# Optimization experiments

Measured on AMD Instinct MI355X. Metric: run time of the kernel, lower is better.

## Reference

```python
import jax, jax.numpy as jnp
import numpy as np

BLOCK_LEN = 64

def _segsum(x):
    # x: (..., T) -> (..., T, T) with entry [t, s] = sum_{u=s+1..t} x[u], -inf above diagonal
    T = x.shape[-1]
    cs = jnp.cumsum(x, axis=-1)
    ss = cs[..., :, None] - cs[..., None, :]
    mask = jnp.tril(jnp.ones((T, T), dtype=bool))
    return jnp.where(mask, ss, -jnp.inf)

def setup_inputs() -> dict:
    key = jax.random.key(0)
    kx, ka, kb, kc = jax.random.split(key, 4)
    b, L, h, p, n = 4, 4096, 32, 64, 16
    X = jax.random.normal(kx, (b, L, h, p), dtype=jnp.float32)
    # negative, small-magnitude A so exp(cumsum(A)) stays finite (decaying SSM),
    # matching the math of the module while keeping the baseline numerically sane
    A = -0.1 * jnp.abs(jax.random.normal(ka, (b, L, h), dtype=jnp.float32))
    B = jax.random.normal(kb, (b, L, h, n), dtype=jnp.float32)
    C = jax.random.normal(kc, (b, L, h, n), dtype=jnp.float32)
    return {"X": X, "A": A, "B": B, "C": C}

def reference(X, A, B, C):
    b, L, h, p = X.shape
    n = B.shape[-1]
    l = BLOCK_LEN
    c = L // l
    # chunk into blocks
    Xb = X.reshape(b, c, l, h, p)                       # b c l h p
    Ab = A.reshape(b, c, l, h).transpose(0, 3, 1, 2)    # b h c l
    Bb = B.reshape(b, c, l, h, n)                       # b c l h n
    Cb = C.reshape(b, c, l, h, n)                       # b c l h n
    A_cumsum = jnp.cumsum(Ab, axis=-1)                  # b h c l
    # intra-chunk (diagonal) term; equals the fused per-timestep scan
    # h_t = exp(A_t)*h_{t-1} + B_t*x_t ; y_t = C_t . h_t
    Lmat = jnp.exp(_segsum(Ab))                         # b h c l l (lower-tri)
    Y_diag = jnp.einsum('bclhn,bcshn,bhcls,bcshp->bclhp', Cb, Bb, Lmat, Xb)
    # per-chunk end states
    decay_states = jnp.exp(A_cumsum[..., -1:] - A_cumsum)  # b h c l
    states = jnp.einsum('bclhn,bhcl,bclhp->bchpn', Bb, decay_states, Xb)
    states = jnp.concatenate([jnp.zeros_like(states[:, :1]), states], axis=1)  # b (c+1) h p n
    # inter-chunk recurrence via segment-sum of chunk totals
    decay_chunk = jnp.exp(_segsum(jnp.pad(A_cumsum[..., -1], ((0, 0), (0, 0), (1, 0)))))  # b h (c+1) (c+1)
    new_states = jnp.einsum('bhzc,bchpn->bzhpn', decay_chunk, states)
    states = new_states[:, :-1]                          # b c h p n
    # state -> output contribution
    state_decay_out = jnp.exp(A_cumsum)                  # b h c l
    Y_off = jnp.einsum('bclhn,bchpn,bhcl->bclhp', Cb, states, state_decay_out)
    return (Y_diag + Y_off).reshape(b, L, h, p)
```

## Files before the change

### kernel.cpp

```cpp
#include <hip/hip_runtime.h>

#define BATCH   4
#define SEQLEN  4096
#define NHEADS  32
#define PDIM    64
#define NDIM    16
#define CHUNK   64
#define NCHUNK  64

typedef short v8s __attribute__((ext_vector_type(8)));
typedef float v4f __attribute__((ext_vector_type(4)));

__device__ __forceinline__ short f2bf(float f) {
    union { float f; unsigned u; } x; x.f = f;
    unsigned r = (x.u + 0x7FFFu + ((x.u >> 16) & 1u)) >> 16;
    return (short)r;
}
__device__ __forceinline__ float bf2f(short s) {
    union { unsigned u; float f; } x; x.u = ((unsigned)(unsigned short)s) << 16;
    return x.f;
}

__device__ __forceinline__ float wave_iscan(float v, int lane) {
#pragma unroll
    for (int d = 1; d < 64; d <<= 1) {
        float o = __shfl_up(v, (unsigned)d, 64);
        if (lane >= d) v += o;
    }
    return v;
}

__global__ __launch_bounds__(256) void k_states(
    const float* __restrict__ X, const float* __restrict__ A,
    const float* __restrict__ Bm, float* __restrict__ states,
    float* __restrict__ csum)
{
    const int cc = blockIdx.x, hh = blockIdx.y, bb = blockIdx.z;
    const int tid = threadIdx.x;
    const int lane = tid & 63, W = tid >> 6;
    const int t0 = bb * SEQLEN + cc * CHUNK;

    __shared__ __align__(16) float sXraw[CHUNK][PDIM + 1];
    __shared__ __align__(16) short bF[1024];
    __shared__ float sDec[CHUNK];

    {
        const int sb = tid >> 4, p4 = (tid & 15) * 4;
        for (int i = 0; i < 4; ++i) {
            int s = sb + i * 16;
            const float4 v = *(const float4*)&X[((size_t)(t0 + s) * NHEADS + hh) * PDIM + p4];
            sXraw[s][p4]     = v.x; sXraw[s][p4 + 1] = v.y;
            sXraw[s][p4 + 2] = v.z; sXraw[s][p4 + 3] = v.w;
        }
    }
    {
        const int r = tid >> 2, n0 = (tid & 3) * 4;
        float4 bv = *(const float4*)&Bm[((size_t)(t0 + r) * NHEADS + hh) * NDIM + n0];
        const int kk = r >> 5, q = (r >> 3) & 3, j = r & 7;
        const int base = (kk * 64 + q * 16) * 8 + j;
        bF[base + (n0 + 0) * 8] = f2bf(bv.x);
        bF[base + (n0 + 1) * 8] = f2bf(bv.y);
        bF[base + (n0 + 2) * 8] = f2bf(bv.z);
        bF[base + (n0 + 3) * 8] = f2bf(bv.w);
    }
    if (tid < 64) {
        float a = A[(t0 + tid) * NHEADS + hh];
        float v = wave_iscan(a, lane);
        float tot = __shfl(v, 63, 64);
        sDec[tid] = __expf(tot - v);
        if (tid == 0) csum[(bb * NHEADS + hh) * NCHUNK + cc] = tot;
    }
    __syncthreads();

    const int m = lane & 15, q = lane >> 4;
    v8s a0, a1;
#pragma unroll
    for (int j = 0; j < 8; ++j) {
        const int tr = q * 8 + j;
        a0[j] = f2bf(sXraw[tr][W * 16 + m] * sDec[tr]);
        a1[j] = f2bf(sXraw[32 + tr][W * 16 + m] * sDec[32 + tr]);
    }
    v8s b0 = *(const v8s*)&bF[(0 * 64 + lane) * 8];
    v8s b1 = *(const v8s*)&bF[(1 * 64 + lane) * 8];
    const v4f zero = {0.f, 0.f, 0.f, 0.f};
    v4f acc = __builtin_amdgcn_mfma_f32_16x16x32_bf16(a0, b0, zero, 0, 0, 0);
    acc = __builtin_amdgcn_mfma_f32_16x16x32_bf16(a1, b1, acc, 0, 0, 0);

    const int n = lane & 15;
    float* sp = states + ((size_t)(bb * NHEADS + hh) * NCHUNK + cc) * (PDIM * NDIM);
#pragma unroll
    for (int r = 0; r < 4; ++r)
        sp[(W * 16 + q * 4 + r) * NDIM + n] = acc[r];
}

__global__ __launch_bounds__(256) void k_scan(
    float* __restrict__ states, const float* __restrict__ csum)
{
    const int bh = blockIdx.y;
    const int el = blockIdx.x * 256 + threadIdx.x;
    __shared__ float sE[NCHUNK];
    if (threadIdx.x < NCHUNK) sE[threadIdx.x] = __expf(csum[bh * NCHUNK + threadIdx.x]);
    __syncthreads();
    float* base = states + (size_t)bh * NCHUNK * (PDIM * NDIM) + el;
    float v[NCHUNK];
#pragma unroll
    for (int z = 0; z < NCHUNK; ++z) v[z] = base[z * (PDIM * NDIM)];
    float S = 0.f;
#pragma unroll
    for (int z = 0; z < NCHUNK; ++z) {
        const float nv = v[z];
        v[z] = S;
        S = sE[z] * S + nv;
    }
#pragma unroll
    for (int z = 0; z < NCHUNK; ++z) base[z * (PDIM * NDIM)] = v[z];
}

__global__ __launch_bounds__(256) void k_out(
    const float* __restrict__ X, const float* __restrict__ A,
    const float* __restrict__ Bm, const float* __restrict__ Cm,
    const float* __restrict__ states, float* __restrict__ Y)
{
    const int cc = blockIdx.x, hh = blockIdx.y, bb = blockIdx.z;
    const int tid = threadIdx.x;
    const int lane = tid & 63, W = tid >> 6;
    const int qq = lane >> 4, nn = lane & 15;
    const int t0 = bb * SEQLEN + cc * CHUNK;

    __shared__ __align__(16) char uBuf[CHUNK * (PDIM + 1) * 4];
    float (*sXraw)[PDIM + 1] = (float (*)[PDIM + 1])uBuf;
    short* gF = (short*)uBuf;
    __shared__ __align__(16) short xF[4096];
    __shared__ __align__(16) short cF[2048];
    __shared__ __align__(16) short bF[2048];
    __shared__ __align__(16) short sF[2048];
    __shared__ float sCum[CHUNK];

    {
        const int sb = tid >> 4, p4 = (tid & 15) * 4;
        for (int i = 0; i < 4; ++i) {
            int s = sb + i * 16;
            const float4 v = *(const float4*)&X[((size_t)(t0 + s) * NHEADS + hh) * PDIM + p4];
            sXraw[s][p4]     = v.x; sXraw[s][p4 + 1] = v.y;
            sXraw[s][p4 + 2] = v.z; sXraw[s][p4 + 3] = v.w;
        }
    }
    {
        const int r = tid >> 2, nn0 = (tid & 3) * 4;
        const int off = ((r >> 4) * 64 + (nn0 >> 3) * 16 + (r & 15)) * 8 + (nn0 & 7);
        float4 cv = *(const float4*)&Cm[((size_t)(t0 + r) * NHEADS + hh) * NDIM + nn0];
        cF[off] = f2bf(cv.x); cF[off + 1] = f2bf(cv.y);
        cF[off + 2] = f2bf(cv.z); cF[off + 3] = f2bf(cv.w);
        float4 bv = *(const float4*)&Bm[((size_t)(t0 + r) * NHEADS + hh) * NDIM + nn0];
        bF[off] = f2bf(bv.x); bF[off + 1] = f2bf(bv.y);
        bF[off + 2] = f2bf(bv.z); bF[off + 3] = f2bf(bv.w);
        const float* sp = states + ((size_t)(bb * NHEADS + hh) * NCHUNK + cc) * (PDIM * NDIM)
                                 + r * NDIM + nn0;
        float4 sv = *(const float4*)sp;
        sF[off] = f2bf(sv.x); sF[off + 1] = f2bf(sv.y);
        sF[off + 2] = f2bf(sv.z); sF[off + 3] = f2bf(sv.w);
    }
    {
        const v8s z8 = {0, 0, 0, 0, 0, 0, 0, 0};
        for (int z = tid; z < 384; z += 256) {
            short* base = (z < 128) ? cF : (z < 256) ? bF : sF;
            int idx = z & 127;
            int off = (idx >> 5) * 512 + 256 + (idx & 31) * 8;
            *(v8s*)&base[off] = z8;
        }
    }
    if (tid < 64) {
        float a = A[(t0 + tid) * NHEADS + hh];
        sCum[tid] = wave_iscan(a, lane);
    }
    __syncthreads();

    for (int c = tid; c < 512; c += 256) {
        int cn = c & 15, cq = (c >> 4) & 3, nt = (c >> 6) & 3, kk = c >> 8;
        int srow = kk * 32 + cq * 8, p = nt * 16 + cn;
        v8s v;
        for (int j = 0; j < 8; ++j) v[j] = f2bf(sXraw[srow + j][p]);
        *(v8s*)&xF[c * 8] = v;
    }
    __syncthreads();

    const v8s cfrag = *(const v8s*)&cF[(W * 64 + lane) * 8];
    const v4f zero = {0.f, 0.f, 0.f, 0.f};
    for (int st = 0; st < 4; ++st) {
        const int kk = st >> 1, q2 = (st & 1) * 2 + (nn >> 3), j2 = nn & 7;
        if (st <= W) {
            v8s bfrag = *(const v8s*)&bF[(st * 64 + lane) * 8];
            v4f acc = __builtin_amdgcn_mfma_f32_16x16x32_bf16(cfrag, bfrag, zero, 0, 0, 0);
            const int s = st * 16 + nn;
            const float cums = sCum[s];
            for (int r = 0; r < 4; ++r) {
                int t = W * 16 + qq * 4 + r;
                float g = (t >= s) ? acc[r] * __expf(sCum[t] - cums) : 0.f;
                gF[((W * 2 + kk) * 64 + q2 * 16 + qq * 4 + r) * 8 + j2] = f2bf(g);
            }
        } else if (kk == 0 || W >= 2) {
            for (int r = 0; r < 4; ++r)
                gF[((W * 2 + kk) * 64 + q2 * 16 + qq * 4 + r) * 8 + j2] = 0;
        }
    }
    const float et = __expf(sCum[W * 16 + nn]);
    v8s cefrag;
    for (int j = 0; j < 8; ++j) cefrag[j] = f2bf(bf2f(cfrag[j]) * et);
    __syncthreads();

    const v8s ga0 = *(const v8s*)&gF[((W * 2 + 0) * 64 + lane) * 8];
    const bool usekk1 = (W >= 2);
    v8s ga1 = {0, 0, 0, 0, 0, 0, 0, 0};
    if (usekk1) ga1 = *(const v8s*)&gF[((W * 2 + 1) * 64 + lane) * 8];
    v4f acc[4];
    for (int nt = 0; nt < 4; ++nt) {
        v8s sfrag = *(const v8s*)&sF[(nt * 64 + lane) * 8];
        v4f a = __builtin_amdgcn_mfma_f32_16x16x32_bf16(cefrag, sfrag, zero, 0, 0, 0);
        v8s x0 = *(const v8s*)&xF[((0 * 4 + nt) * 64 + lane) * 8];
        a = __builtin_amdgcn_mfma_f32_16x16x32_bf16(ga0, x0, a, 0, 0, 0);
        if (usekk1) {
            v8s x1 = *(const v8s*)&xF[((1 * 4 + nt) * 64 + lane) * 8];
            a = __builtin_amdgcn_mfma_f32_16x16x32_bf16(ga1, x1, a, 0, 0, 0);
        }
        acc[nt] = a;
    }
    for (int r = 0; r < 4; ++r) {
        int t = W * 16 + qq * 4 + r;
        float* yp = Y + ((size_t)(t0 + t) * NHEADS + hh) * PDIM + nn;
        for (int nt = 0; nt < 4; ++nt) yp[nt * 16] = acc[nt][r];
    }
}

extern "C" void kernel_launch(void* const* d_in, const int* in_sizes, int n_in,
                              void* d_out, int out_size, void* d_ws, size_t ws_size,
                              hipStream_t stream) {
    const float* X  = (const float*)d_in[0];
    const float* A  = (const float*)d_in[1];
    const float* Bm = (const float*)d_in[2];
    const float* Cm = (const float*)d_in[3];
    float* Y = (float*)d_out;

    float* states = (float*)d_ws;
    float* csum   = states + (size_t)BATCH * NHEADS * NCHUNK * PDIM * NDIM;

    dim3 grid(NCHUNK, NHEADS, BATCH);
    k_states<<<grid, 256, 0, stream>>>(X, A, Bm, states, csum);
    dim3 gscan(4, BATCH * NHEADS, 1);
    k_scan<<<gscan, 256, 0, stream>>>(states, csum);
    k_out<<<grid, 256, 0, stream>>>(X, A, Bm, Cm, states, Y);
}
```

Measured before the change: 335.0 us.

## Fuse state, scan and output kernels into one chunk-sequential double-buffered kernel

Replaces the three-kernel pipeline (per-chunk states, inter-chunk scan, output) with a single kernel in which each block owns one (batch, head, half of P) slice and walks the 64 chunks in order. The inter-chunk state is carried in registers and handed to the next chunk through shared memory, so the global workspace write and read of chunk states disappears. Four producer waves prefetch the next chunk's X, B, C and A into double-buffered shared memory while four consumer waves compute the current chunk. The cost is much less parallelism: only 256 blocks, each running a 64-step serial loop with a block barrier per step, so speed depends on hiding global load latency within each block.

```diff
diff --git a/kernel.cpp b/kernel.cpp
--- a/kernel.cpp
+++ b/kernel.cpp
@@ -7,6 +7,7 @@
 #define NDIM    16
 #define CHUNK   64
 #define NCHUNK  64
+#define PHALF   32
 
 typedef short v8s __attribute__((ext_vector_type(8)));
 typedef float v4f __attribute__((ext_vector_type(4)));
@@ -30,204 +31,162 @@
     return v;
 }
 
-__global__ __launch_bounds__(256) void k_states(
+__global__ __launch_bounds__(512) void k_fused(
     const float* __restrict__ X, const float* __restrict__ A,
-    const float* __restrict__ Bm, float* __restrict__ states,
-    float* __restrict__ csum)
+    const float* __restrict__ Bm, const float* __restrict__ Cm,
+    float* __restrict__ Y)
 {
-    const int cc = blockIdx.x, hh = blockIdx.y, bb = blockIdx.z;
+    const int ph = blockIdx.x, hh = blockIdx.y, bb = blockIdx.z;
     const int tid = threadIdx.x;
-    const int lane = tid & 63, W = tid >> 6;
-    const int t0 = bb * SEQLEN + cc * CHUNK;
-
-    __shared__ __align__(16) float sXraw[CHUNK][PDIM + 1];
-    __shared__ __align__(16) short bF[1024];
-    __shared__ float sDec[CHUNK];
+    const int lane = tid & 63;
+    const int wv = tid >> 6;
+    const int W = wv & 3;
+    const int qq = lane >> 4, nn = lane & 15;
+
+    __shared__ __align__(16) float sXraw[2][CHUNK][PHALF + 1];
+    __shared__ __align__(16) short cFq[2][2048];
+    __shared__ __align__(16) short bFq[2][2048];
+    __shared__ __align__(16) short bFs[2][1024];
+    __shared__ __align__(16) short sF [2][1024];
+    __shared__ __align__(16) short gF [4096];
+    __shared__ float araw[2][CHUNK];
 
     {
-        const int sb = tid >> 4, p4 = (tid & 15) * 4;
-        for (int i = 0; i < 4; ++i) {
-            int s = sb + i * 16;
-            const float4 v = *(const float4*)&X[((size_t)(t0 + s) * NHEADS + hh) * PDIM + p4];
-            sXraw[s][p4]     = v.x; sXraw[s][p4 + 1] = v.y;
-            sXraw[s][p4 + 2] = v.z; sXraw[s][p4 + 3] = v.w;
-        }
-    }
-    {
-        const int r = tid >> 2, n0 = (tid & 3) * 4;
-        float4 bv = *(const float4*)&Bm[((size_t)(t0 + r) * NHEADS + hh) * NDIM + n0];
-        const int kk = r >> 5, q = (r >> 3) & 3, j = r & 7;
-        const int base = (kk * 64 + q * 16) * 8 + j;
-        bF[base + (n0 + 0) * 8] = f2bf(bv.x);
-        bF[base + (n0 + 1) * 8] = f2bf(bv.y);
-        bF[base + (n0 + 2) * 8] = f2bf(bv.z);
-        bF[base + (n0 + 3) * 8] = f2bf(bv.w);
-    }
-    if (tid < 64) {
-        float a = A[(t0 + tid) * NHEADS + hh];
-        float v = wave_iscan(a, lane);
-        float tot = __shfl(v, 63, 64);
-        sDec[tid] = __expf(tot - v);
-        if (tid == 0) csum[(bb * NHEADS + hh) * NCHUNK + cc] = tot;
+        const v8s z8 = {0,0,0,0,0,0,0,0};
+        if (tid < 512) { ((v8s*)cFq)[tid] = z8; ((v8s*)bFq)[tid] = z8; }
+        if (tid < 256) ((v8s*)sF)[tid] = z8;
     }
     __syncthreads();
 
-    const int m = lane & 15, q = lane >> 4;
-    v8s a0, a1;
-#pragma unroll
-    for (int j = 0; j < 8; ++j) {
-        const int tr = q * 8 + j;
-        a0[j] = f2bf(sXraw[tr][W * 16 + m] * sDec[tr]);
-        a1[j] = f2bf(sXraw[32 + tr][W * 16 + m] * sDec[32 + tr]);
-    }
-    v8s b0 = *(const v8s*)&bF[(0 * 64 + lane) * 8];
-    v8s b1 = *(const v8s*)&bF[(1 * 64 + lane) * 8];
+    auto stage = [&](int c, int buf) {
+        const int ptid = tid & 255;
+        const int t0c = bb * SEQLEN + c * CHUNK;
+#pragma unroll
+        for (int i = 0; i < 2; ++i) {
+            const int idx = ptid + i * 256;
+            const int row = idx >> 3, p4 = (idx & 7) * 4;
+            const float4 v = *(const float4*)&X[((size_t)(t0c + row) * NHEADS + hh) * PDIM + ph * PHALF + p4];
+            sXraw[buf][row][p4 + 0] = v.x; sXraw[buf][row][p4 + 1] = v.y;
+            sXraw[buf][row][p4 + 2] = v.z; sXraw[buf][row][p4 + 3] = v.w;
+        }
+        {
+            const int r = ptid >> 2, n0 = (ptid & 3) * 4;
+            const float4 bv = *(const float4*)&Bm[((size_t)(t0c + r) * NHEADS + hh) * NDIM + n0];
+            const int offq = ((r >> 4) * 64 + (n0 >> 3) * 16 + (r & 15)) * 8 + (n0 & 7);
+            bFq[buf][offq + 0] = f2bf(bv.x); bFq[buf][offq + 1] = f2bf(bv.y);
+            bFq[buf][offq + 2] = f2bf(bv.z); bFq[buf][offq + 3] = f2bf(bv.w);
+            const int kk = r >> 5, q = (r >> 3) & 3, jj = r & 7;
+            const int bs = (kk * 64 + q * 16) * 8 + jj;
+            bFs[buf][bs + (n0 + 0) * 8] = f2bf(bv.x);
+            bFs[buf][bs + (n0 + 1) * 8] = f2bf(bv.y);
+            bFs[buf][bs + (n0 + 2) * 8] = f2bf(bv.z);
+            bFs[buf][bs + (n0 + 3) * 8] = f2bf(bv.w);
+            const float4 cv = *(const float4*)&Cm[((size_t)(t0c + r) * NHEADS + hh) * NDIM + n0];
+            cFq[buf][offq + 0] = f2bf(cv.x); cFq[buf][offq + 1] = f2bf(cv.y);
+            cFq[buf][offq + 2] = f2bf(cv.z); cFq[buf][offq + 3] = f2bf(cv.w);
+        }
+        if (ptid < CHUNK) araw[buf][ptid] = A[(size_t)(t0c + ptid) * NHEADS + hh];
+    };
+
+    if (wv >= 4) stage(0, 0);
+    __syncthreads();
+
+    v4f S = {0.f, 0.f, 0.f, 0.f};
     const v4f zero = {0.f, 0.f, 0.f, 0.f};
-    v4f acc = __builtin_amdgcn_mfma_f32_16x16x32_bf16(a0, b0, zero, 0, 0, 0);
-    acc = __builtin_amdgcn_mfma_f32_16x16x32_bf16(a1, b1, acc, 0, 0, 0);
-
-    const int n = lane & 15;
-    float* sp = states + ((size_t)(bb * NHEADS + hh) * NCHUNK + cc) * (PDIM * NDIM);
-#pragma unroll
-    for (int r = 0; r < 4; ++r)
-        sp[(W * 16 + q * 4 + r) * NDIM + n] = acc[r];
-}
-
-__global__ __launch_bounds__(256) void k_scan(
-    float* __restrict__ states, const float* __restrict__ csum)
-{
-    const int bh = blockIdx.y;
-    const int el = blockIdx.x * 256 + threadIdx.x;
-    __shared__ float sE[NCHUNK];
-    if (threadIdx.x < NCHUNK) sE[threadIdx.x] = __expf(csum[bh * NCHUNK + threadIdx.x]);
-    __syncthreads();
-    float* base = states + (size_t)bh * NCHUNK * (PDIM * NDIM) + el;
-    float v[NCHUNK];
-#pragma unroll
-    for (int z = 0; z < NCHUNK; ++z) v[z] = base[z * (PDIM * NDIM)];
-    float S = 0.f;
-#pragma unroll
-    for (int z = 0; z < NCHUNK; ++z) {
-        const float nv = v[z];
-        v[z] = S;
-        S = sE[z] * S + nv;
-    }
-#pragma unroll
-    for (int z = 0; z < NCHUNK; ++z) base[z * (PDIM * NDIM)] = v[z];
-}
-
-__global__ __launch_bounds__(256) void k_out(
-    const float* __restrict__ X, const float* __restrict__ A,
-    const float* __restrict__ Bm, const float* __restrict__ Cm,
-    const float* __restrict__ states, float* __restrict__ Y)
-{
-    const int cc = blockIdx.x, hh = blockIdx.y, bb = blockIdx.z;
-    const int tid = threadIdx.x;
-    const int lane = tid & 63, W = tid >> 6;
-    const int qq = lane >> 4, nn = lane & 15;
-    const int t0 = bb * SEQLEN + cc * CHUNK;
-
-    __shared__ __align__(16) char uBuf[CHUNK * (PDIM + 1) * 4];
-    float (*sXraw)[PDIM + 1] = (float (*)[PDIM + 1])uBuf;
-    short* gF = (short*)uBuf;
-    __shared__ __align__(16) short xF[4096];
-    __shared__ __align__(16) short cF[2048];
-    __shared__ __align__(16) short bF[2048];
-    __shared__ __align__(16) short sF[2048];
-    __shared__ float sCum[CHUNK];
-
-    {
-        const int sb = tid >> 4, p4 = (tid & 15) * 4;
-        for (int i = 0; i < 4; ++i) {
-            int s = sb + i * 16;
-            const float4 v = *(const float4*)&X[((size_t)(t0 + s) * NHEADS + hh) * PDIM + p4];
-            sXraw[s][p4]     = v.x; sXraw[s][p4 + 1] = v.y;
-            sXraw[s][p4 + 2] = v.z; sXraw[s][p4 + 3] = v.w;
+
+#pragma unroll 1
+    for (int k = 0; k < NCHUNK; ++k) {
+        const int cur = k & 1;
+        if (wv >= 4) {
+            if (k + 1 < NCHUNK) stage(k + 1, cur ^ 1);
+        } else {
+            const int t0c = bb * SEQLEN + k * CHUNK;
+            const float cum = wave_iscan(araw[cur][lane], lane);
+            const float tot = __shfl(cum, 63, 64);
+            float tcum[4];
+#pragma unroll
+            for (int r = 0; r < 4; ++r) tcum[r] = __shfl(cum, W * 16 + qq * 4 + r, 64);
+
+            const v8s cfrag = *(const v8s*)&cFq[cur][(W * 64 + lane) * 8];
+#pragma unroll
+            for (int st = 0; st < 4; ++st) {
+                const int kk = st >> 1, q2 = (st & 1) * 2 + (nn >> 3), j2 = nn & 7;
+                if (st <= W) {
+                    const v8s bfrag = *(const v8s*)&bFq[cur][(st * 64 + lane) * 8];
+                    v4f acc = __builtin_amdgcn_mfma_f32_16x16x32_bf16(cfrag, bfrag, zero, 0, 0, 0);
+                    const float cums = __shfl(cum, st * 16 + nn, 64);
+#pragma unroll
+                    for (int r = 0; r < 4; ++r) {
+                        const int t = W * 16 + qq * 4 + r;
+                        const int s = st * 16 + nn;
+                        const float g = (t >= s) ? acc[r] * __expf(tcum[r] - cums) : 0.f;
+                        gF[((W * 2 + kk) * 64 + q2 * 16 + qq * 4 + r) * 8 + j2] = f2bf(g);
+                    }
+                } else if (kk == 0 || W >= 2) {
+#pragma unroll
+                    for (int r = 0; r < 4; ++r)
+                        gF[((W * 2 + kk) * 64 + q2 * 16 + qq * 4 + r) * 8 + j2] = 0;
+                }
+            }
+            const float et = __expf(__shfl(cum, W * 16 + nn, 64));
+            v8s cefrag;
+#pragma unroll
+            for (int j = 0; j < 8; ++j) cefrag[j] = f2bf(bf2f(cfrag[j]) * et);
+
+            const v8s ga0 = *(const v8s*)&gF[((W * 2 + 0) * 64 + lane) * 8];
+            const bool usekk1 = (W >= 2);
+            v8s ga1 = {0, 0, 0, 0, 0, 0, 0, 0};
+            if (usekk1) ga1 = *(const v8s*)&gF[((W * 2 + 1) * 64 + lane) * 8];
+
+            v4f ya[2];
+#pragma unroll
+            for (int nt = 0; nt < 2; ++nt) {
+                const v8s sfrag = *(const v8s*)&sF[cur][(nt * 64 + lane) * 8];
+                v4f a = __builtin_amdgcn_mfma_f32_16x16x32_bf16(cefrag, sfrag, zero, 0, 0, 0);
+                v8s x0;
+#pragma unroll
+                for (int j = 0; j < 8; ++j) x0[j] = f2bf(sXraw[cur][qq * 8 + j][nt * 16 + nn]);
+                a = __builtin_amdgcn_mfma_f32_16x16x32_bf16(ga0, x0, a, 0, 0, 0);
+                if (usekk1) {
+                    v8s x1;
+#pragma unroll
+                    for (int j = 0; j < 8; ++j) x1[j] = f2bf(sXraw[cur][32 + qq * 8 + j][nt * 16 + nn]);
+                    a = __builtin_amdgcn_mfma_f32_16x16x32_bf16(ga1, x1, a, 0, 0, 0);
+                }
+                ya[nt] = a;
+            }
+#pragma unroll
+            for (int r = 0; r < 4; ++r) {
+                const int t = W * 16 + qq * 4 + r;
+                float* yp = Y + ((size_t)(t0c + t) * NHEADS + hh) * PDIM + ph * PHALF + nn;
+                yp[0]  = ya[0][r];
+                yp[16] = ya[1][r];
+            }
+
+            if (W < 2) {
+                v8s a0, a1;
+#pragma unroll
+                for (int j = 0; j < 8; ++j) {
+                    const int tr = qq * 8 + j;
+                    a0[j] = f2bf(sXraw[cur][tr][W * 16 + nn] *
+                                 __expf(tot - __shfl(cum, tr, 64)));
+                    a1[j] = f2bf(sXraw[cur][32 + tr][W * 16 + nn] *
+                                 __expf(tot - __shfl(cum, 32 + tr, 64)));
+                }
+                const v8s b0 = *(const v8s*)&bFs[cur][(0 * 64 + lane) * 8];
+                const v8s b1 = *(const v8s*)&bFs[cur][(1 * 64 + lane) * 8];
+                v4f sa = __builtin_amdgcn_mfma_f32_16x16x32_bf16(a0, b0, zero, 0, 0, 0);
+                sa = __builtin_amdgcn_mfma_f32_16x16x32_bf16(a1, b1, sa, 0, 0, 0);
+                const float Et = __expf(tot);
+#pragma unroll
+                for (int r = 0; r < 4; ++r) S[r] = Et * S[r] + sa[r];
+                short* d = &sF[cur ^ 1][0];
+#pragma unroll
+                for (int r = 0; r < 4; ++r)
+                    d[(W * 64 + (nn >> 3) * 16 + qq * 4 + r) * 8 + (nn & 7)] = f2bf(S[r]);
+            }
         }
-    }
-    {
-        const int r = tid >> 2, nn0 = (tid & 3) * 4;
-        const int off = ((r >> 4) * 64 + (nn0 >> 3) * 16 + (r & 15)) * 8 + (nn0 & 7);
-        float4 cv = *(const float4*)&Cm[((size_t)(t0 + r) * NHEADS + hh) * NDIM + nn0];
-        cF[off] = f2bf(cv.x); cF[off + 1] = f2bf(cv.y);
-        cF[off + 2] = f2bf(cv.z); cF[off + 3] = f2bf(cv.w);
-        float4 bv = *(const float4*)&Bm[((size_t)(t0 + r) * NHEADS + hh) * NDIM + nn0];
-        bF[off] = f2bf(bv.x); bF[off + 1] = f2bf(bv.y);
-        bF[off + 2] = f2bf(bv.z); bF[off + 3] = f2bf(bv.w);
-        const float* sp = states + ((size_t)(bb * NHEADS + hh) * NCHUNK + cc) * (PDIM * NDIM)
-                                 + r * NDIM + nn0;
-        float4 sv = *(const float4*)sp;
-        sF[off] = f2bf(sv.x); sF[off + 1] = f2bf(sv.y);
-        sF[off + 2] = f2bf(sv.z); sF[off + 3] = f2bf(sv.w);
-    }
-    {
-        const v8s z8 = {0, 0, 0, 0, 0, 0, 0, 0};
-        for (int z = tid; z < 384; z += 256) {
-            short* base = (z < 128) ? cF : (z < 256) ? bF : sF;
-            int idx = z & 127;
-            int off = (idx >> 5) * 512 + 256 + (idx & 31) * 8;
-            *(v8s*)&base[off] = z8;
-        }
-    }
-    if (tid < 64) {
-        float a = A[(t0 + tid) * NHEADS + hh];
-        sCum[tid] = wave_iscan(a, lane);
-    }
-    __syncthreads();
-
-    for (int c = tid; c < 512; c += 256) {
-        int cn = c & 15, cq = (c >> 4) & 3, nt = (c >> 6) & 3, kk = c >> 8;
-        int srow = kk * 32 + cq * 8, p = nt * 16 + cn;
-        v8s v;
-        for (int j = 0; j < 8; ++j) v[j] = f2bf(sXraw[srow + j][p]);
-        *(v8s*)&xF[c * 8] = v;
-    }
-    __syncthreads();
-
-    const v8s cfrag = *(const v8s*)&cF[(W * 64 + lane) * 8];
-    const v4f zero = {0.f, 0.f, 0.f, 0.f};
-    for (int st = 0; st < 4; ++st) {
-        const int kk = st >> 1, q2 = (st & 1) * 2 + (nn >> 3), j2 = nn & 7;
-        if (st <= W) {
-            v8s bfrag = *(const v8s*)&bF[(st * 64 + lane) * 8];
-            v4f acc = __builtin_amdgcn_mfma_f32_16x16x32_bf16(cfrag, bfrag, zero, 0, 0, 0);
-            const int s = st * 16 + nn;
-            const float cums = sCum[s];
-            for (int r = 0; r < 4; ++r) {
-                int t = W * 16 + qq * 4 + r;
-                float g = (t >= s) ? acc[r] * __expf(sCum[t] - cums) : 0.f;
-                gF[((W * 2 + kk) * 64 + q2 * 16 + qq * 4 + r) * 8 + j2] = f2bf(g);
-            }
-        } else if (kk == 0 || W >= 2) {
-            for (int r = 0; r < 4; ++r)
-                gF[((W * 2 + kk) * 64 + q2 * 16 + qq * 4 + r) * 8 + j2] = 0;
-        }
-    }
-    const float et = __expf(sCum[W * 16 + nn]);
-    v8s cefrag;
-    for (int j = 0; j < 8; ++j) cefrag[j] = f2bf(bf2f(cfrag[j]) * et);
-    __syncthreads();
-
-    const v8s ga0 = *(const v8s*)&gF[((W * 2 + 0) * 64 + lane) * 8];
-    const bool usekk1 = (W >= 2);
-    v8s ga1 = {0, 0, 0, 0, 0, 0, 0, 0};
-    if (usekk1) ga1 = *(const v8s*)&gF[((W * 2 + 1) * 64 + lane) * 8];
-    v4f acc[4];
-    for (int nt = 0; nt < 4; ++nt) {
-        v8s sfrag = *(const v8s*)&sF[(nt * 64 + lane) * 8];
-        v4f a = __builtin_amdgcn_mfma_f32_16x16x32_bf16(cefrag, sfrag, zero, 0, 0, 0);
-        v8s x0 = *(const v8s*)&xF[((0 * 4 + nt) * 64 + lane) * 8];
-        a = __builtin_amdgcn_mfma_f32_16x16x32_bf16(ga0, x0, a, 0, 0, 0);
-        if (usekk1) {
-            v8s x1 = *(const v8s*)&xF[((1 * 4 + nt) * 64 + lane) * 8];
-            a = __builtin_amdgcn_mfma_f32_16x16x32_bf16(ga1, x1, a, 0, 0, 0);
-        }
-        acc[nt] = a;
-    }
-    for (int r = 0; r < 4; ++r) {
-        int t = W * 16 + qq * 4 + r;
-        float* yp = Y + ((size_t)(t0 + t) * NHEADS + hh) * PDIM + nn;
-        for (int nt = 0; nt < 4; ++nt) yp[nt * 16] = acc[nt][r];
+        __syncthreads();
     }
 }
 
@@ -239,13 +198,8 @@
     const float* Bm = (const float*)d_in[2];
     const float* Cm = (const float*)d_in[3];
     float* Y = (float*)d_out;
-
-    float* states = (float*)d_ws;
-    float* csum   = states + (size_t)BATCH * NHEADS * NCHUNK * PDIM * NDIM;
-
-    dim3 grid(NCHUNK, NHEADS, BATCH);
-    k_states<<<grid, 256, 0, stream>>>(X, A, Bm, states, csum);
-    dim3 gscan(4, BATCH * NHEADS, 1);
-    k_scan<<<gscan, 256, 0, stream>>>(states, csum);
-    k_out<<<grid, 256, 0, stream>>>(X, A, Bm, Cm, states, Y);
-}
+    (void)d_ws; (void)ws_size;
+
+    dim3 grid(2, NHEADS, BATCH);
+    k_fused<<<grid, 512, 0, stream>>>(X, A, Bm, Cm, Y);
+}
```

New measurement: 398.6 us. +19.0%, slower.
